# Performance work log

Measured on AMD Instinct MI355X. Metric: run time of the kernel, lower is better.

The kernel has to match this reference:

```python
import jax, jax.numpy as jnp
import numpy as np


def setup_inputs() -> dict:
    key = jax.random.key(0)
    ks = jax.random.split(key, 7)
    B, C, L, A = 8, 1024, 2048, 128
    x = jax.random.normal(ks[0], (B, C, L), dtype=jnp.float32)
    Wk = jax.random.normal(ks[1], (A, C), dtype=jnp.float32) * (1.0 / np.sqrt(C))
    bk = jax.random.normal(ks[2], (A,), dtype=jnp.float32) * 0.01
    Wq = jax.random.normal(ks[3], (A, C), dtype=jnp.float32) * (1.0 / np.sqrt(C))
    bq = jax.random.normal(ks[4], (A,), dtype=jnp.float32) * 0.01
    Wp = jax.random.normal(ks[5], (C, C), dtype=jnp.float32) * (1.0 / np.sqrt(C))
    bp = jax.random.normal(ks[6], (C,), dtype=jnp.float32) * 0.01
    return {"x": x, "Wk": Wk, "bk": bk, "Wq": Wq, "bq": bq, "Wp": Wp, "bp": bp}


def reference(x, Wk, bk, Wq, bq, Wp, bp):
    # x: [B, C, L]; 1x1 Conv1d == pointwise linear over channel dim
    keys = jnp.einsum('bcl,ac->bal', x, Wk) + bk[None, :, None]      # [B, A, L]
    queries = jnp.einsum('bcl,ac->bal', x, Wq) + bq[None, :, None]   # [B, A, L]
    values = jnp.einsum('bal,bam->blm', keys, queries)               # keys^T @ queries -> [B, L, L]
    seqlen = x.shape[2]
    # NOTE: source uses seqlen ** 1 / 2 which is seqlen/2 due to Python precedence
    attn = jax.nn.softmax(values / (seqlen / 2.0), axis=-1)          # [B, L, L]
    out = jnp.einsum('bcl,blm->bcm', x, attn)                        # x @ attn -> [B, C, L]
    out = jnp.einsum('bcm,dc->bdm', out, Wp) + bp[None, :, None]     # output projection
    return out
```

## Files before the change

### kernel.cpp

```cpp
#include <hip/hip_runtime.h>
#include <hip/hip_bf16.h>

typedef __hip_bfloat16 bf16;
typedef __attribute__((ext_vector_type(8))) short bfrag8;
typedef __attribute__((ext_vector_type(8))) int intx8;
typedef __attribute__((ext_vector_type(4))) float floatx4;


__device__ __forceinline__ unsigned char f2fp8(float f) {
    f = fminf(fmaxf(f, -448.f), 448.f);
    return (unsigned char)(__builtin_amdgcn_cvt_pk_fp8_f32(f, f, 0, false) & 0xFF);
}

__device__ __forceinline__ void async_copy16(const void* g, void* lds) {
    __builtin_amdgcn_global_load_lds(
        (const __attribute__((address_space(1))) unsigned int*)g,
        (__attribute__((address_space(3))) unsigned int*)lds, 16, 0, 0);
}

template<int BIASMODE, int OUTKIND, bool EXPZ, bool MFAST>
__global__ __launch_bounds__(256)
void gemm128(const bf16* __restrict__ Ag, long sAb, int lda,
             const bf16* __restrict__ Bg, long sBb, int ldb,
             void* __restrict__ Cg, long sCb, int ldc,
             const float* __restrict__ scl, const float* __restrict__ b2,
             float* __restrict__ Zp, int K, int logfast)
{
    __shared__ unsigned short As[128 * 64];
    __shared__ unsigned short Bs[128 * 64];

    const int lin = blockIdx.x;
    const int bz  = lin & 7;
    const int s   = lin >> 3;
    const int msk = (1 << logfast) - 1;
    int mT, nT;
    if (MFAST) { mT = s & msk; nT = s >> logfast; }
    else       { nT = s & msk; mT = s >> logfast; }

    const bf16* A  = Ag + (size_t)bz * sAb + (size_t)mT * 128 * lda;
    const bf16* Bp = Bg + (size_t)bz * sBb + (size_t)nT * 128 * ldb;
    const int t = threadIdx.x, wave = t >> 6, lane = t & 63;
    const int qrow = lane & 15, quad = lane >> 4;
    const int wr = (wave >> 1) * 64, wc = (wave & 1) * 64;

    floatx4 acc[4][4] = {};

    for (int k0 = 0; k0 < K; k0 += 64) {
        #pragma unroll
        for (int j = 0; j < 4; ++j) {
            int c = j * 256 + t;
            int r = c >> 3, p = c & 7;
            int g = p ^ (r & 7);
            async_copy16(A + (size_t)r * lda + k0 + g * 8, &As[c * 8]);
        }
        #pragma unroll
        for (int j = 0; j < 4; ++j) {
            int c = j * 256 + t;
            int r = c >> 3, p = c & 7;
            int g = p ^ (r & 7);
            async_copy16(Bp + (size_t)r * ldb + k0 + g * 8, &Bs[c * 8]);
        }
        __syncthreads();

        #pragma unroll
        for (int ks = 0; ks < 2; ++ks) {
            bfrag8 af[4], bfv[4];
            #pragma unroll
            for (int mi = 0; mi < 4; ++mi) {
                int row = wr + mi * 16 + qrow;
                int ck  = ks * 4 + quad;
                af[mi] = *(const bfrag8*)&As[row * 64 + ((ck ^ (row & 7)) * 8)];
            }
            #pragma unroll
            for (int ni = 0; ni < 4; ++ni) {
                int row = wc + ni * 16 + qrow;
                int ck  = ks * 4 + quad;
                bfv[ni] = *(const bfrag8*)&Bs[row * 64 + ((ck ^ (row & 7)) * 8)];
            }
            #pragma unroll
            for (int mi = 0; mi < 4; ++mi)
                #pragma unroll
                for (int ni = 0; ni < 4; ++ni)
                    acc[mi][ni] = __builtin_amdgcn_mfma_f32_16x16x32_bf16(
                        af[mi], bfv[ni], acc[mi][ni], 0, 0, 0);
        }
        __syncthreads();
    }

    const int bmr = mT * 128 + wr, bnc = nT * 128 + wc;
    float zp[4] = {0.f, 0.f, 0.f, 0.f};
    #pragma unroll
    for (int mi = 0; mi < 4; ++mi) {
        #pragma unroll
        for (int ni = 0; ni < 4; ++ni) {
            int col = bnc + ni * 16 + qrow;
            #pragma unroll
            for (int r = 0; r < 4; ++r) {
                int row = bmr + mi * 16 + quad * 4 + r;
                float v = acc[mi][ni][r];
                if (EXPZ) { float e = __expf(v); zp[ni] += e; v = (e - 1.0f) * 4096.0f; }
                if (BIASMODE == 1) v = v * scl[col] + b2[col];
                if (BIASMODE == 2) v += scl[row];
                if (OUTKIND == 1)
                    ((float*)Cg + (size_t)bz * sCb)[(size_t)row * ldc + col] = v;
                else if (OUTKIND == 0)
                    ((bf16*)Cg + (size_t)bz * sCb)[(size_t)row * ldc + col] = __float2bfloat16(v);
                else
                    ((unsigned char*)Cg + (size_t)bz * sCb)[(size_t)row * ldc + col] = f2fp8(v);
            }
        }
    }
    if (EXPZ) {
        #pragma unroll
        for (int ni = 0; ni < 4; ++ni) {
            float tt = zp[ni];
            tt += __shfl_xor(tt, 16, 64);
            tt += __shfl_xor(tt, 32, 64);
            if (quad == 0)
                atomicAdd(&Zp[bz * 2048 + bnc + ni * 16 + qrow], tt);
        }
    }
}

template<int MODE, bool MFAST>
__global__ __launch_bounds__(512, 2)
void gemm_f8(const unsigned char* __restrict__ Ag, long sAb, int lda,
             const unsigned char* __restrict__ Bg, long sBb, int ldb,
             void* __restrict__ Cg, long sCb, int ldc,
             const float* __restrict__ rowb, float os, int K, int logfast)
{
    __shared__ __align__(16) unsigned char smem[131072];

    const int lin = blockIdx.x;
    const int bz  = lin & 7;
    const int s0  = lin >> 3;
    const int msk = (1 << logfast) - 1;
    int mT, nT;
    if (MFAST) { mT = s0 & msk; nT = s0 >> logfast; }
    else       { nT = s0 & msk; mT = s0 >> logfast; }

    const unsigned char* A  = Ag + (size_t)bz * sAb + (size_t)mT * 256 * lda;
    const unsigned char* Bp = Bg + (size_t)bz * sBb + (size_t)nT * 256 * ldb;
    const int t = threadIdx.x, wave = t >> 6, lane = t & 63;
    const int qrow = lane & 15, quad = lane >> 4;
    const int wm = (wave >> 2) * 128;
    const int wn = (wave & 3) * 64;

    floatx4 acc[8][4] = {};

    auto stage = [&](int kt, int slot) {
        const int k0 = kt << 7;
        unsigned char* Ad = &smem[slot * 32768];
        unsigned char* Bd = &smem[65536 + slot * 32768];
        #pragma unroll
        for (int j = 0; j < 4; ++j) {
            int c = j * 512 + t;
            int r = c >> 3, p = c & 7, g = p ^ (r & 7);
            async_copy16(A + (size_t)r * lda + k0 + g * 16, Ad + c * 16);
        }
        #pragma unroll
        for (int j = 0; j < 4; ++j) {
            int c = j * 512 + t;
            int r = c >> 3, p = c & 7, g = p ^ (r & 7);
            async_copy16(Bp + (size_t)r * ldb + k0 + g * 16, Bd + c * 16);
        }
    };

    const int NT = K >> 7;
    stage(0, 0);
    stage(1, 1);

    for (int kt = 0; kt < NT; ++kt) {
        const int slot = kt & 1;
        if (kt + 1 < NT) asm volatile("s_waitcnt vmcnt(8)" ::: "memory");
        else             asm volatile("s_waitcnt vmcnt(0)" ::: "memory");
        __builtin_amdgcn_sched_barrier(0);
        __builtin_amdgcn_s_barrier();
        __builtin_amdgcn_sched_barrier(0);

        const unsigned char* As = &smem[slot * 32768];
        const unsigned char* Bs = &smem[65536 + slot * 32768];

        intx8 bfr[4];
        #pragma unroll
        for (int ni = 0; ni < 4; ++ni) {
            int row = wn + ni * 16 + qrow, sw = row & 7;
            union { intx8 v; uint4 q[2]; } u;
            u.q[0] = *(const uint4*)&Bs[row * 128 + (((quad * 2    ) ^ sw) * 16)];
            u.q[1] = *(const uint4*)&Bs[row * 128 + (((quad * 2 + 1) ^ sw) * 16)];
            bfr[ni] = u.v;
        }
        #pragma unroll
        for (int mi = 0; mi < 8; ++mi) {
            int row = wm + mi * 16 + qrow, sw = row & 7;
            union { intx8 v; uint4 q[2]; } u;
            u.q[0] = *(const uint4*)&As[row * 128 + (((quad * 2    ) ^ sw) * 16)];
            u.q[1] = *(const uint4*)&As[row * 128 + (((quad * 2 + 1) ^ sw) * 16)];
            intx8 af = u.v;
            #pragma unroll
            for (int ni = 0; ni < 4; ++ni)
                acc[mi][ni] = __builtin_amdgcn_mfma_scale_f32_16x16x128_f8f6f4(
                    af, bfr[ni], acc[mi][ni], 0, 0, 0, 127, 0, 127);
        }

        __builtin_amdgcn_sched_barrier(0);
        __builtin_amdgcn_s_barrier();
        __builtin_amdgcn_sched_barrier(0);
        if (kt + 2 < NT) stage(kt + 2, slot);
    }

    const int bmr = mT * 256 + wm, bnc = nT * 256 + wn;
    #pragma unroll
    for (int mi = 0; mi < 8; ++mi) {
        int row0 = bmr + mi * 16 + quad * 4;
        float4 rb4;
        if (MODE == 2) rb4 = *(const float4*)&rowb[bz * 1024 + row0];
        #pragma unroll
        for (int ni = 0; ni < 4; ++ni) {
            int col = bnc + ni * 16 + qrow;
            floatx4 a = acc[mi][ni];
            if (MODE == 2) {
                float* Co = (float*)Cg + (size_t)bz * sCb;
                Co[(size_t)(row0 + 0) * ldc + col] = a[0] * os + rb4.x;
                Co[(size_t)(row0 + 1) * ldc + col] = a[1] * os + rb4.y;
                Co[(size_t)(row0 + 2) * ldc + col] = a[2] * os + rb4.z;
                Co[(size_t)(row0 + 3) * ldc + col] = a[3] * os + rb4.w;
            } else {
                unsigned char* C8 = (unsigned char*)Cg + (size_t)bz * sCb;
                #pragma unroll
                for (int r = 0; r < 4; ++r)
                    C8[(size_t)(row0 + r) * ldc + col] = f2fp8(a[r] * os);
            }
        }
    }
}

__global__ __launch_bounds__(256)
void conv_w(const float* __restrict__ Wk, const float* __restrict__ Wq,
            const float* __restrict__ Wp, bf16* __restrict__ Wkqb,
            unsigned char* __restrict__ Wp8)
{
    int i = blockIdx.x * 256 + threadIdx.x;
    if (i < 32768) {
        const float* src = (i < 16384) ? Wk : Wq;
        int off = (i < 16384) ? i : i - 16384;
        bf16* dst = Wkqb + (size_t)((i < 16384) ? 0 : 131072);
        const float4* sp = (const float4*)src + (size_t)off * 2;
        float4 a = sp[0], b = sp[1];
        union { uint4 u; unsigned short h[8]; } o;
        union { bf16 h; unsigned short u; } cv;
        cv.h = __float2bfloat16(a.x); o.h[0] = cv.u;
        cv.h = __float2bfloat16(a.y); o.h[1] = cv.u;
        cv.h = __float2bfloat16(a.z); o.h[2] = cv.u;
        cv.h = __float2bfloat16(a.w); o.h[3] = cv.u;
        cv.h = __float2bfloat16(b.x); o.h[4] = cv.u;
        cv.h = __float2bfloat16(b.y); o.h[5] = cv.u;
        cv.h = __float2bfloat16(b.z); o.h[6] = cv.u;
        cv.h = __float2bfloat16(b.w); o.h[7] = cv.u;
        ((uint4*)dst)[off] = o.u;
    } else {
        int off = i - 32768;
        const float4* sp = (const float4*)Wp + (size_t)off * 2;
        float4 a = sp[0], b = sp[1];
        unsigned char o[8];
        o[0] = f2fp8(a.x * 2048.f); o[1] = f2fp8(a.y * 2048.f);
        o[2] = f2fp8(a.z * 2048.f); o[3] = f2fp8(a.w * 2048.f);
        o[4] = f2fp8(b.x * 2048.f); o[5] = f2fp8(b.y * 2048.f);
        o[6] = f2fp8(b.z * 2048.f); o[7] = f2fp8(b.w * 2048.f);
        uint2 w;
        w.x = (unsigned int)o[0] | ((unsigned int)o[1] << 8) | ((unsigned int)o[2] << 16) | ((unsigned int)o[3] << 24);
        w.y = (unsigned int)o[4] | ((unsigned int)o[5] << 8) | ((unsigned int)o[6] << 16) | ((unsigned int)o[7] << 24);
        ((uint2*)Wp8)[off] = w;
    }
}

__global__ __launch_bounds__(256)
void conv_x(const float* __restrict__ x, bf16* __restrict__ xt)
{
    const int b = blockIdx.z;
    const int l0 = blockIdx.x * 64, c0 = blockIdx.y * 64;
    const float* xp = x + (size_t)b * 1024 * 2048;
    bf16* xtp = xt + (size_t)b * 2048 * 1024;
    __shared__ unsigned short tile[64][65];
    const int t = threadIdx.x, tr = t >> 4, tc4 = (t & 15) * 4;
    union { bf16 h; unsigned short u; } cv;
    #pragma unroll
    for (int i = 0; i < 4; ++i) {
        int r = i * 16 + tr;
        float4 v = *(const float4*)(xp + (size_t)(c0 + r) * 2048 + l0 + tc4);
        cv.h = __float2bfloat16(v.x); tile[r][tc4]     = cv.u;
        cv.h = __float2bfloat16(v.y); tile[r][tc4 + 1] = cv.u;
        cv.h = __float2bfloat16(v.z); tile[r][tc4 + 2] = cv.u;
        cv.h = __float2bfloat16(v.w); tile[r][tc4 + 3] = cv.u;
    }
    __syncthreads();
    #pragma unroll
    for (int i = 0; i < 4; ++i) {
        int lr = i * 16 + tr;
        union { uint2 u; unsigned short h[4]; } o;
        #pragma unroll
        for (int j = 0; j < 4; ++j) o.h[j] = tile[tc4 + j][lr];
        *(uint2*)(xtp + (size_t)(l0 + lr) * 1024 + c0 + tc4) = o.u;
    }
}

__global__ void prep_bias(const float* __restrict__ bk, const float* __restrict__ bq,
                          float* __restrict__ scl, float* __restrict__ b2, float kscale)
{
    int t = threadIdx.x;
    float s = (t < 128) ? kscale : 1.0f;
    scl[t] = s;
    b2[t] = ((t < 128) ? bk[t] : bq[t - 128]) * s;
}

__global__ __launch_bounds__(256)
void normx(const float* __restrict__ x, const float* __restrict__ Z,
           unsigned char* __restrict__ xs, float* __restrict__ colsum)
{
    const int bc = blockIdx.x;
    const int b  = bc >> 10;
    const int t  = threadIdx.x;
    const float* xp = x + (size_t)bc * 2048 + t * 8;
    const float* zp = Z + b * 2048 + t * 8;
    float4 a = ((const float4*)xp)[0], c4 = ((const float4*)xp)[1];
    float4 z0 = ((const float4*)zp)[0], z1 = ((const float4*)zp)[1];
    float v[8];
    v[0] = a.x  / fmaxf(z0.x, 1e-10f); v[1] = a.y / fmaxf(z0.y, 1e-10f);
    v[2] = a.z  / fmaxf(z0.z, 1e-10f); v[3] = a.w / fmaxf(z0.w, 1e-10f);
    v[4] = c4.x / fmaxf(z1.x, 1e-10f); v[5] = c4.y / fmaxf(z1.y, 1e-10f);
    v[6] = c4.z / fmaxf(z1.z, 1e-10f); v[7] = c4.w / fmaxf(z1.w, 1e-10f);
    float s = 0.f;
    unsigned char o[8];
    #pragma unroll
    for (int j = 0; j < 8; ++j) { s += v[j]; o[j] = f2fp8(v[j] * 65536.f); }
    uint2 w;
    w.x = (unsigned int)o[0] | ((unsigned int)o[1] << 8) | ((unsigned int)o[2] << 16) | ((unsigned int)o[3] << 24);
    w.y = (unsigned int)o[4] | ((unsigned int)o[5] << 8) | ((unsigned int)o[6] << 16) | ((unsigned int)o[7] << 24);
    ((uint2*)(xs + (size_t)bc * 2048))[t] = w;
    #pragma unroll
    for (int off = 32; off >= 1; off >>= 1) s += __shfl_xor(s, off, 64);
    __shared__ float red[4];
    if ((t & 63) == 0) red[t >> 6] = s;
    __syncthreads();
    if (t == 0) colsum[bc] = red[0] + red[1] + red[2] + red[3];
}

__global__ __launch_bounds__(256)
void basek(const float* __restrict__ Wp, const float* __restrict__ colsum,
           const float* __restrict__ bp, float* __restrict__ base)
{
    const int d = blockIdx.x, t = threadIdx.x;
    float4 w = *(const float4*)(Wp + (size_t)d * 1024 + t * 4);
    float pb[8];
    #pragma unroll
    for (int b = 0; b < 8; ++b) {
        float4 cs = *(const float4*)(colsum + b * 1024 + t * 4);
        pb[b] = w.x * cs.x + w.y * cs.y + w.z * cs.z + w.w * cs.w;
    }
    __shared__ float red[8][4];
    #pragma unroll
    for (int b = 0; b < 8; ++b) {
        float s = pb[b];
        #pragma unroll
        for (int off = 32; off >= 1; off >>= 1) s += __shfl_xor(s, off, 64);
        if ((t & 63) == 0) red[b][t >> 6] = s;
    }
    __syncthreads();
    if (t < 8) base[t * 1024 + d] = bp[d] + red[t][0] + red[t][1] + red[t][2] + red[t][3];
}

extern "C" void kernel_launch(void* const* d_in, const int* in_sizes, int n_in,
                              void* d_out, int out_size, void* d_ws, size_t ws_size,
                              hipStream_t stream)
{
    const float* x  = (const float*)d_in[0];
    const float* Wk = (const float*)d_in[1];
    const float* bk = (const float*)d_in[2];
    const float* Wq = (const float*)d_in[3];
    const float* bq = (const float*)d_in[4];
    const float* Wp = (const float*)d_in[5];
    const float* bp = (const float*)d_in[6];
    float* out = (float*)d_out;

    const float kscale = 2.0f / 2048.0f;

    bf16* xt   = (bf16*)d_ws;
    bf16* KQt  = xt + (size_t)8 * 2048 * 1024;
    bf16* Wkqb = KQt + (size_t)8 * 2048 * 256;
    unsigned char* Wp8 = (unsigned char*)(Wkqb + (size_t)256 * 1024);
    unsigned char* St8 = Wp8 + (size_t)1048576;
    unsigned char* xs8 = St8 + (size_t)8 * 2048 * 2048;
    float* Z      = (float*)(xs8 + (size_t)8 * 1024 * 2048);
    float* colsum = Z + 8 * 2048;
    float* base   = colsum + 8 * 1024;
    float* scl    = base + 8 * 1024;
    float* b2     = scl + 256;
    unsigned char* Dlt = (unsigned char*)xt;

    dim3 blk(256, 1, 1);
    dim3 blk512(512, 1, 1);

    prep_bias<<<dim3(1), blk, 0, stream>>>(bk, bq, scl, b2, kscale);
    conv_w<<<dim3(640), blk, 0, stream>>>(Wk, Wq, Wp, Wkqb, Wp8);
    conv_x<<<dim3(32, 16, 8), blk, 0, stream>>>(x, xt);

    gemm128<1, 0, false, false><<<dim3(8 * 16 * 2), blk, 0, stream>>>(
        xt, 2048L * 1024, 1024,  Wkqb, 0, 1024,
        KQt, 2048L * 256, 256,  scl, b2, nullptr, 1024, 1);

    hipMemsetAsync(Z, 0, (size_t)8 * 2048 * sizeof(float), stream);

    gemm128<0, 2, true, false><<<dim3(8 * 16 * 16), blk, 0, stream>>>(
        KQt + 128, 2048L * 256, 256,  KQt, 2048L * 256, 256,
        St8, 2048L * 2048, 2048,  nullptr, nullptr, Z, 128, 4);

    normx<<<dim3(8 * 1024), blk, 0, stream>>>(x, Z, xs8, colsum);
    basek<<<dim3(1024), blk, 0, stream>>>(Wp, colsum, bp, base);

    gemm_f8<0, false><<<dim3(8 * 8 * 4), blk512, 0, stream>>>(
        St8, 2048L * 2048, 2048,  xs8, 1024L * 2048, 2048,
        Dlt, 2048L * 1024, 1024,  nullptr, 0.0009765625f, 2048, 2);

    gemm_f8<2, true><<<dim3(8 * 4 * 8), blk512, 0, stream>>>(
        Wp8, 0, 1024,  Dlt, 2048L * 1024, 1024,
        out, 1024L * 2048, 2048,  base, 1.862645149230957e-9f, 1024, 2);
}
```

Measured before the change: 262.0 us.

## Interleave next-tile async loads with MFMA phases in fp8 GEMM main loop

Restructures the fp8 GEMM k-loop into four phases per tile. The next tile's global-to-LDS copies are issued in halves during the first two phases instead of prefetching two tiles ahead. Each phase adds barriers and raises wave priority around its MFMA block, aiming to overlap loads with compute and keep the matrix cores busy. The cost is a shallower prefetch depth, since it now waits with vmcnt(0) each tile, plus more block-level barriers per tile, which could expose more memory latency.

```diff
diff --git a/kernel.cpp b/kernel.cpp
--- a/kernel.cpp
+++ b/kernel.cpp
@@ -148,65 +148,88 @@
 
     floatx4 acc[8][4] = {};
 
-    auto stage = [&](int kt, int slot) {
+    auto stage_part = [&](int kt, int slot, int part) {
         const int k0 = kt << 7;
         unsigned char* Ad = &smem[slot * 32768];
         unsigned char* Bd = &smem[65536 + slot * 32768];
         #pragma unroll
-        for (int j = 0; j < 4; ++j) {
-            int c = j * 512 + t;
+        for (int j = 0; j < 2; ++j) {
+            int c = (part * 2 + j) * 512 + t;
             int r = c >> 3, p = c & 7, g = p ^ (r & 7);
             async_copy16(A + (size_t)r * lda + k0 + g * 16, Ad + c * 16);
         }
         #pragma unroll
-        for (int j = 0; j < 4; ++j) {
-            int c = j * 512 + t;
+        for (int j = 0; j < 2; ++j) {
+            int c = (part * 2 + j) * 512 + t;
             int r = c >> 3, p = c & 7, g = p ^ (r & 7);
             async_copy16(Bp + (size_t)r * ldb + k0 + g * 16, Bd + c * 16);
         }
     };
 
     const int NT = K >> 7;
-    stage(0, 0);
-    stage(1, 1);
+    stage_part(0, 0, 0);
+    stage_part(0, 0, 1);
 
     for (int kt = 0; kt < NT; ++kt) {
         const int slot = kt & 1;
-        if (kt + 1 < NT) asm volatile("s_waitcnt vmcnt(8)" ::: "memory");
-        else             asm volatile("s_waitcnt vmcnt(0)" ::: "memory");
+        const unsigned char* As = &smem[slot * 32768];
+        const unsigned char* Bs = &smem[65536 + slot * 32768];
+
+        asm volatile("s_waitcnt vmcnt(0)" ::: "memory");
         __builtin_amdgcn_sched_barrier(0);
         __builtin_amdgcn_s_barrier();
         __builtin_amdgcn_sched_barrier(0);
 
-        const unsigned char* As = &smem[slot * 32768];
-        const unsigned char* Bs = &smem[65536 + slot * 32768];
-
         intx8 bfr[4];
         #pragma unroll
-        for (int ni = 0; ni < 4; ++ni) {
-            int row = wn + ni * 16 + qrow, sw = row & 7;
-            union { intx8 v; uint4 q[2]; } u;
-            u.q[0] = *(const uint4*)&Bs[row * 128 + (((quad * 2    ) ^ sw) * 16)];
-            u.q[1] = *(const uint4*)&Bs[row * 128 + (((quad * 2 + 1) ^ sw) * 16)];
-            bfr[ni] = u.v;
-        }
-        #pragma unroll
-        for (int mi = 0; mi < 8; ++mi) {
-            int row = wm + mi * 16 + qrow, sw = row & 7;
-            union { intx8 v; uint4 q[2]; } u;
-            u.q[0] = *(const uint4*)&As[row * 128 + (((quad * 2    ) ^ sw) * 16)];
-            u.q[1] = *(const uint4*)&As[row * 128 + (((quad * 2 + 1) ^ sw) * 16)];
-            intx8 af = u.v;
+        for (int ph = 0; ph < 4; ++ph) {
+            if (ph == 0) {
+                #pragma unroll
+                for (int ni = 0; ni < 4; ++ni) {
+                    int row = wn + ni * 16 + qrow, sw = row & 7;
+                    union { intx8 v; uint4 q[2]; } u;
+                    u.q[0] = *(const uint4*)&Bs[row * 128 + (((quad * 2    ) ^ sw) * 16)];
+                    u.q[1] = *(const uint4*)&Bs[row * 128 + (((quad * 2 + 1) ^ sw) * 16)];
+                    bfr[ni] = u.v;
+                }
+            }
+            intx8 af0, af1;
+            {
+                int row = wm + (2 * ph) * 16 + qrow, sw = row & 7;
+                union { intx8 v; uint4 q[2]; } u;
+                u.q[0] = *(const uint4*)&As[row * 128 + (((quad * 2    ) ^ sw) * 16)];
+                u.q[1] = *(const uint4*)&As[row * 128 + (((quad * 2 + 1) ^ sw) * 16)];
+                af0 = u.v;
+            }
+            {
+                int row = wm + (2 * ph + 1) * 16 + qrow, sw = row & 7;
+                union { intx8 v; uint4 q[2]; } u;
+                u.q[0] = *(const uint4*)&As[row * 128 + (((quad * 2    ) ^ sw) * 16)];
+                u.q[1] = *(const uint4*)&As[row * 128 + (((quad * 2 + 1) ^ sw) * 16)];
+                af1 = u.v;
+            }
+            if (ph < 2 && kt + 1 < NT) stage_part(kt + 1, slot ^ 1, ph);
+
+            __builtin_amdgcn_sched_barrier(0);
+            __builtin_amdgcn_s_barrier();
+            asm volatile("s_waitcnt lgkmcnt(0)" ::: "memory");
+            __builtin_amdgcn_sched_barrier(0);
+
+            __builtin_amdgcn_s_setprio(1);
             #pragma unroll
             for (int ni = 0; ni < 4; ++ni)
-                acc[mi][ni] = __builtin_amdgcn_mfma_scale_f32_16x16x128_f8f6f4(
-                    af, bfr[ni], acc[mi][ni], 0, 0, 0, 127, 0, 127);
-        }
-
-        __builtin_amdgcn_sched_barrier(0);
-        __builtin_amdgcn_s_barrier();
-        __builtin_amdgcn_sched_barrier(0);
-        if (kt + 2 < NT) stage(kt + 2, slot);
+                acc[2 * ph][ni] = __builtin_amdgcn_mfma_scale_f32_16x16x128_f8f6f4(
+                    af0, bfr[ni], acc[2 * ph][ni], 0, 0, 0, 127, 0, 127);
+            #pragma unroll
+            for (int ni = 0; ni < 4; ++ni)
+                acc[2 * ph + 1][ni] = __builtin_amdgcn_mfma_scale_f32_16x16x128_f8f6f4(
+                    af1, bfr[ni], acc[2 * ph + 1][ni], 0, 0, 0, 127, 0, 127);
+            __builtin_amdgcn_s_setprio(0);
+
+            __builtin_amdgcn_sched_barrier(0);
+            __builtin_amdgcn_s_barrier();
+            __builtin_amdgcn_sched_barrier(0);
+        }
     }
 
     const int bmr = mT * 256 + wm, bnc = nT * 256 + wn;
```

Result: no change. 260.2 us (-0.7%).
